# Optimization experiments

Hardware: AMD Instinct MI355X
Metric: run time of the kernel (lower is better)

Reference implementation:

```python
import jax, jax.numpy as jnp
import numpy as np

B, L, D, H, DK = 4, 256, 512, 8, 64
NEG_INF = 1.0e9


def setup_inputs() -> dict:
    key = jax.random.key(0)
    ks = jax.random.split(key, 12)
    s = 1.0 / np.sqrt(D)
    inp = {
        "q": jax.random.normal(ks[0], (B, L, D), jnp.float32),
        "k": jax.random.normal(ks[1], (B, L, D), jnp.float32),
        "v": jax.random.normal(ks[2], (B, L, D), jnp.float32),
        "mask": jnp.ones((B, L, L), jnp.int32),
        "Wq": jax.random.normal(ks[3], (D, D), jnp.float32) * s,
        "bq": jnp.zeros((D,), jnp.float32),
        "Wk": jax.random.normal(ks[4], (D, D), jnp.float32) * s,
        "bk": jnp.zeros((D,), jnp.float32),
        "Wv": jax.random.normal(ks[5], (D, D), jnp.float32) * s,
        "bv": jnp.zeros((D,), jnp.float32),
        "vp": jax.random.normal(ks[6], (1, H, 1, 1, DK), jnp.float32) * 0.1,
        "W0": jax.random.normal(ks[7], (D, D), jnp.float32) * s,
        "b0": jnp.zeros((D,), jnp.float32),
    }
    return inp


def reference(q, k, v, mask, Wq, bq, Wk, bk, Wv, bv, vp, W0, b0):
    # project and split heads: (B, L, D) -> (B, H, L, DK)
    qh = (q @ Wq + bq).reshape(B, L, H, DK).transpose(0, 2, 1, 3)
    kh = (k @ Wk + bk).reshape(B, L, H, DK).transpose(0, 2, 1, 3)
    vh = (v @ Wv + bv).reshape(B, L, H, DK).transpose(0, 2, 1, 3)
    # additive (Bahdanau) scoring: (B, H, Lq, Lk, DK) intermediate
    energy = jnp.tanh(qh[:, :, :, None, :] + kh[:, :, None, :, :])
    scores = jnp.sum(vp * energy, axis=-1)  # (B, H, Lq, Lk)
    scores = jnp.where(mask[:, None] == 0, -NEG_INF, scores)
    attn = jax.nn.softmax(scores, axis=-1)
    out = jnp.matmul(attn, vh)  # (B, H, Lq, DK)
    out = out.transpose(0, 2, 1, 3).reshape(B, L, D)
    return out @ W0 + b0
```

## Files before the change

### kernel.cpp

```cpp
#include <hip/hip_runtime.h>

#define LSEQ 256
#define DMODEL 512
#define NHEAD 8
#define DKH 64
#define BATCH 4

#define TWO_LOG2E 2.885390081777927f

using short8 = __attribute__((ext_vector_type(8))) short;
using f32x4  = __attribute__((ext_vector_type(4))) float;

__device__ __forceinline__ void split4(const float* f, ushort4& h, ushort4& l) {
  unsigned short hh[4], ll[4];
#pragma unroll
  for (int j = 0; j < 4; ++j) {
    unsigned int u = __float_as_uint(f[j]);
    hh[j] = (unsigned short)(u >> 16);
    float hf = __uint_as_float(u & 0xFFFF0000u);
    ll[j] = (unsigned short)(__float_as_uint(f[j] - hf) >> 16);
  }
  h = make_ushort4(hh[0], hh[1], hh[2], hh[3]);
  l = make_ushort4(ll[0], ll[1], ll[2], ll[3]);
}

__global__ __launch_bounds__(256) void prep_kernel(
    const float* __restrict__ q, const float* __restrict__ k, const float* __restrict__ v,
    const float* __restrict__ Wq, const float* __restrict__ Wk,
    const float* __restrict__ Wv, const float* __restrict__ W0,
    unsigned short* __restrict__ xhi, unsigned short* __restrict__ xlo,
    unsigned short* __restrict__ whi, unsigned short* __restrict__ wlo)
{
  const int z = blockIdx.z;
  const int tid = threadIdx.x;
  if (z < 3) {
    const float* X = (z == 0) ? q : (z == 1) ? k : v;
    const int r = blockIdx.x * 32 + (tid >> 3);
    const int c = blockIdx.y * 32 + ((tid & 7) << 2);
    float4 f = *(const float4*)&X[r * DMODEL + c];
    ushort4 h4, l4;
    split4((const float*)&f, h4, l4);
    const int base = (z * 1024 + r) * DMODEL + c;
    *(ushort4*)&xhi[base] = h4;
    *(ushort4*)&xlo[base] = l4;
  } else {
    if (blockIdx.x >= 16) return;
    const int g = z - 3;
    const float* W = (g == 0) ? Wq : (g == 1) ? Wk : (g == 2) ? Wv : W0;
    const float scale = (g < 2) ? TWO_LOG2E : 1.0f;
    const int k0 = blockIdx.x * 32, n0 = blockIdx.y * 32;
    __shared__ float tile[32][36];
    {
      const int r = tid >> 3, c = (tid & 7) << 2;
      float4 f = *(const float4*)&W[(k0 + r) * DMODEL + n0 + c];
      tile[r][c + 0] = f.x * scale;
      tile[r][c + 1] = f.y * scale;
      tile[r][c + 2] = f.z * scale;
      tile[r][c + 3] = f.w * scale;
    }
    __syncthreads();
    const int n = tid >> 3, kk = (tid & 7) << 2;
    float x[4];
#pragma unroll
    for (int j = 0; j < 4; ++j) x[j] = tile[kk + j][n];
    ushort4 h4, l4;
    split4(x, h4, l4);
    const int base = (g * DMODEL + n0 + n) * DMODEL + k0 + kk;
    *(ushort4*)&whi[base] = h4;
    *(ushort4*)&wlo[base] = l4;
  }
}

__device__ __forceinline__ void mfma_gemm(
    const unsigned short* __restrict__ xh, const unsigned short* __restrict__ xl,
    const unsigned short* __restrict__ wh, const unsigned short* __restrict__ wl,
    const float* __restrict__ bias, float bscale,
    float* __restrict__ out, int mode)
{
  __shared__ short8 ldsT[4][512];
  const int tid = threadIdx.x;
  const int lane = tid & 63, w = tid >> 6;
  const int bm0 = blockIdx.x * 64, bn0 = blockIdx.y * 64;

  const int r0 = tid >> 3, c0 = tid & 7;
  const int g0 = c0 ^ (r0 & 7);
  const int r1 = r0 + 32;
  const int g1 = c0 ^ (r1 & 7);
  const size_t offA0 = (size_t)(bm0 + r0) * DMODEL + g0 * 8;
  const size_t offA1 = (size_t)(bm0 + r1) * DMODEL + g1 * 8;
  const size_t offB0 = (size_t)(bn0 + r0) * DMODEL + g0 * 8;
  const size_t offB1 = (size_t)(bn0 + r1) * DMODEL + g1 * 8;

  const int mrb = (w >> 1) << 5, ncb = (w & 1) << 5;
  const int l15 = lane & 15, lh = lane >> 4, l7 = lane & 7;

  short8 st[8];
#define LOADS(K)                                        \
  { st[0] = *(const short8*)(xh + offA0 + (K));         \
    st[1] = *(const short8*)(xh + offA1 + (K));         \
    st[2] = *(const short8*)(xl + offA0 + (K));         \
    st[3] = *(const short8*)(xl + offA1 + (K));         \
    st[4] = *(const short8*)(wh + offB0 + (K));         \
    st[5] = *(const short8*)(wh + offB1 + (K));         \
    st[6] = *(const short8*)(wl + offB0 + (K));         \
    st[7] = *(const short8*)(wl + offB1 + (K)); }
#define WRITES                                          \
  { ldsT[0][tid] = st[0]; ldsT[0][tid + 256] = st[1];   \
    ldsT[1][tid] = st[2]; ldsT[1][tid + 256] = st[3];   \
    ldsT[2][tid] = st[4]; ldsT[2][tid + 256] = st[5];   \
    ldsT[3][tid] = st[6]; ldsT[3][tid + 256] = st[7]; }

  f32x4 acc[2][2] = {};
  LOADS(0);
  WRITES;
  __syncthreads();

  for (int t = 0; t < 8; ++t) {
    if (t < 7) LOADS((t + 1) * 64);
#pragma unroll
    for (int s = 0; s < 2; ++s) {
      const int chb = (s << 2) + lh;
      const int ra0 = (mrb + l15) * 8 + (chb ^ l7);
      const int ra1 = (mrb + 16 + l15) * 8 + (chb ^ l7);
      const int rb0 = (ncb + l15) * 8 + (chb ^ l7);
      const int rb1 = (ncb + 16 + l15) * 8 + (chb ^ l7);
      short8 a0h = ldsT[0][ra0], a0l = ldsT[1][ra0];
      short8 a1h = ldsT[0][ra1], a1l = ldsT[1][ra1];
      short8 b0h = ldsT[2][rb0], b0l = ldsT[3][rb0];
      short8 b1h = ldsT[2][rb1], b1l = ldsT[3][rb1];
#define MFMA_(A, B, C) C = __builtin_amdgcn_mfma_f32_16x16x32_bf16(A, B, C, 0, 0, 0)
      MFMA_(a0h, b0h, acc[0][0]); MFMA_(a0h, b0l, acc[0][0]); MFMA_(a0l, b0h, acc[0][0]);
      MFMA_(a0h, b1h, acc[0][1]); MFMA_(a0h, b1l, acc[0][1]); MFMA_(a0l, b1h, acc[0][1]);
      MFMA_(a1h, b0h, acc[1][0]); MFMA_(a1h, b0l, acc[1][0]); MFMA_(a1l, b0h, acc[1][0]);
      MFMA_(a1h, b1h, acc[1][1]); MFMA_(a1h, b1l, acc[1][1]); MFMA_(a1l, b1h, acc[1][1]);
#undef MFMA_
    }
    __syncthreads();
    if (t < 7) { WRITES; __syncthreads(); }
  }
#undef LOADS
#undef WRITES

  const int bm = bm0 + mrb, bn = bn0 + ncb;
#pragma unroll
  for (int mi = 0; mi < 2; ++mi)
#pragma unroll
    for (int ni = 0; ni < 2; ++ni) {
      const int C = bn + ni * 16 + l15;
      const float bv = bscale * bias[C];
#pragma unroll
      for (int e = 0; e < 4; ++e) {
        const int R = bm + mi * 16 + (lh << 2) + e;
        const float val = acc[mi][ni][e] + bv;
        if (mode == 0) {
          out[R * DMODEL + C] = val;
        } else {
          const int b = R >> 8, l = R & (LSEQ - 1);
          const int hh = C >> 6, dk = C & 63;
          if (mode == 1) out[((b * NHEAD + hh) * LSEQ + l) * DKH + dk] = val;
          else           out[((b * NHEAD + hh) * DKH + dk) * LSEQ + l] = val;
        }
      }
    }
}

__global__ __launch_bounds__(256) void proj_mfma_kernel(
    const unsigned short* __restrict__ xhi, const unsigned short* __restrict__ xlo,
    const unsigned short* __restrict__ whi, const unsigned short* __restrict__ wlo,
    const float* __restrict__ bq, const float* __restrict__ bk, const float* __restrict__ bv,
    float* __restrict__ qh, float* __restrict__ kT, float* __restrict__ vh)
{
  const int g = blockIdx.z;
  const unsigned short* xh = xhi + (size_t)g * 1024 * DMODEL;
  const unsigned short* xl = xlo + (size_t)g * 1024 * DMODEL;
  const unsigned short* wh = whi + (size_t)g * DMODEL * DMODEL;
  const unsigned short* wl = wlo + (size_t)g * DMODEL * DMODEL;
  if (g == 0)      mfma_gemm(xh, xl, wh, wl, bq, TWO_LOG2E, qh, 1);
  else if (g == 1) mfma_gemm(xh, xl, wh, wl, bk, TWO_LOG2E, kT, 2);
  else             mfma_gemm(xh, xl, wh, wl, bv, 1.0f, vh, 1);
}

__global__ __launch_bounds__(256) void outproj_mfma_kernel(
    const unsigned short* __restrict__ aoh, const unsigned short* __restrict__ aol,
    const unsigned short* __restrict__ whi, const unsigned short* __restrict__ wlo,
    const float* __restrict__ b0, float* __restrict__ out)
{
  mfma_gemm(aoh, aol, whi + (size_t)3 * DMODEL * DMODEL,
            wlo + (size_t)3 * DMODEL * DMODEL, b0, 1.0f, out, 0);
}

__global__ __launch_bounds__(512) void attn_kernel(
    const float* __restrict__ qh,
    const float* __restrict__ kT,
    const float* __restrict__ vh,
    const int* __restrict__ mask,
    const float* __restrict__ vp,
    unsigned short* __restrict__ aoh,
    unsigned short* __restrict__ aol)
{
  __shared__ float ksh[DKH][LSEQ];
  __shared__ float vsh[LSEQ][DKH];
  __shared__ float qsh[32][DKH];
  __shared__ float psh[8][LSEQ];
  __shared__ float vpsh[DKH];

  const int bh = blockIdx.x;
  const int b = bh >> 3, h = bh & 7;
  const int i0 = blockIdx.y * 32;
  const int tid = threadIdx.x;
  const int lane = tid & 63, w = tid >> 6;

  const float* kbase = kT + (size_t)bh * DKH * LSEQ;
  for (int t = tid; t < DKH * LSEQ / 4; t += 512) {
    const int d = t >> 6, j4 = (t & 63) << 2;
    *(float4*)&ksh[d][j4] = *(const float4*)&kbase[d * LSEQ + j4];
  }
  const float* vbase = vh + (size_t)bh * LSEQ * DKH;
  for (int t = tid; t < LSEQ * DKH / 4; t += 512) {
    const int j = t >> 4, d4 = (t & 15) << 2;
    *(float4*)&vsh[j][d4] = *(const float4*)&vbase[j * DKH + d4];
  }
  {
    const float* qbase = qh + ((size_t)bh * LSEQ + i0) * DKH;
    const int r = tid >> 4, d4 = (tid & 15) << 2;
    *(float4*)&qsh[r][d4] = *(const float4*)&qbase[r * DKH + d4];
  }
  if (tid < DKH) vpsh[tid] = vp[h * DKH + tid];
  __syncthreads();

  float tj[4][4] = {};
#pragma unroll 2
  for (int g = 0; g < 16; ++g) {
    float kv[16];
#pragma unroll
    for (int t = 0; t < 4; ++t)
#pragma unroll
      for (int c = 0; c < 4; ++c)
        kv[t * 4 + c] = ksh[(g << 2) + t][(c << 6) + lane];
    float vpv[4];
    *(float4*)vpv = *(const float4*)&vpsh[g << 2];
#pragma unroll
    for (int r = 0; r < 4; ++r) {
      float q_[4];
      *(float4*)q_ = *(const float4*)&qsh[(w << 2) + r][g << 2];
#pragma unroll
      for (int t = 0; t < 4; ++t)
#pragma unroll
        for (int c = 0; c < 4; ++c) {
          const float x = q_[t] + kv[t * 4 + c];
          const float e = __builtin_amdgcn_exp2f(x);
          tj[r][c] = fmaf(vpv[t], __builtin_amdgcn_rcpf(e + 1.f), tj[r][c]);
        }
    }
  }

  const int cg = lane >> 4, qq = lane & 15;
#pragma unroll
  for (int r = 0; r < 4; ++r) {
    const int i = i0 + (w << 2) + r;
    const int* mrow = mask + ((size_t)b * LSEQ + i) * LSEQ;
    float t4[4];
#pragma unroll
    for (int c = 0; c < 4; ++c) {
      const int mv = mrow[(c << 6) + lane];
      t4[c] = mv ? tj[r][c] : 1.0e9f;
    }
    float m = fminf(fminf(t4[0], t4[1]), fminf(t4[2], t4[3]));
#pragma unroll
    for (int off = 32; off; off >>= 1) m = fminf(m, __shfl_xor(m, off));
    const float m2 = m * TWO_LOG2E;
    float p[4];
    float sum = 0.f;
#pragma unroll
    for (int c = 0; c < 4; ++c) {
      p[c] = __builtin_amdgcn_exp2f(fmaf(t4[c], -TWO_LOG2E, m2));
      sum += p[c];
    }
#pragma unroll
    for (int off = 32; off; off >>= 1) sum += __shfl_xor(sum, off);
    const float rs = __builtin_amdgcn_rcpf(sum);
#pragma unroll
    for (int c = 0; c < 4; ++c) psh[w][(c << 6) + lane] = p[c];

    float o[4] = {0.f, 0.f, 0.f, 0.f};
#pragma unroll 4
    for (int jg = 0; jg < 16; ++jg) {
      float pv[4];
      *(float4*)pv = *(const float4*)&psh[w][(cg << 6) + (jg << 2)];
#pragma unroll
      for (int t = 0; t < 4; ++t) {
        float v_[4];
        *(float4*)v_ = *(const float4*)&vsh[(cg << 6) + (jg << 2) + t][qq << 2];
#pragma unroll
        for (int u = 0; u < 4; ++u) o[u] = fmaf(pv[t], v_[u], o[u]);
      }
    }
#pragma unroll
    for (int off = 16; off <= 32; off <<= 1) {
#pragma unroll
      for (int u = 0; u < 4; ++u) o[u] += __shfl_xor(o[u], off);
    }
    if (lane < 16) {
      float ov[4];
#pragma unroll
      for (int u = 0; u < 4; ++u) ov[u] = o[u] * rs;
      ushort4 h4, l4;
      split4(ov, h4, l4);
      const int base = ((size_t)b * LSEQ + i) * DMODEL + h * DKH + (qq << 2);
      *(ushort4*)&aoh[base] = h4;
      *(ushort4*)&aol[base] = l4;
    }
  }
}

extern "C" void kernel_launch(void* const* d_in, const int* in_sizes, int n_in,
                              void* d_out, int out_size, void* d_ws, size_t ws_size,
                              hipStream_t stream) {
  const float* q   = (const float*)d_in[0];
  const float* k   = (const float*)d_in[1];
  const float* v   = (const float*)d_in[2];
  const int*  mask = (const int*)d_in[3];
  const float* Wq  = (const float*)d_in[4];
  const float* bq  = (const float*)d_in[5];
  const float* Wk  = (const float*)d_in[6];
  const float* bk  = (const float*)d_in[7];
  const float* Wv  = (const float*)d_in[8];
  const float* bv  = (const float*)d_in[9];
  const float* vp  = (const float*)d_in[10];
  const float* W0  = (const float*)d_in[11];
  const float* b0  = (const float*)d_in[12];
  float* outp = (float*)d_out;

  char* wsb = (char*)d_ws;
  unsigned short* whi = (unsigned short*)(wsb);
  unsigned short* wlo = (unsigned short*)(wsb + (2u << 20));
  unsigned short* xhi = (unsigned short*)(wsb + (4u << 20));
  unsigned short* xlo = (unsigned short*)(wsb + (7u << 20));
  float* qh = (float*)(wsb + (10u << 20));
  float* kT = (float*)(wsb + (12u << 20));
  float* vh = (float*)(wsb + (14u << 20));
  unsigned short* aoh = xhi;
  unsigned short* aol = xlo;

  prep_kernel<<<dim3(32, 16, 7), 256, 0, stream>>>(q, k, v, Wq, Wk, Wv, W0,
                                                   xhi, xlo, whi, wlo);
  proj_mfma_kernel<<<dim3(16, 8, 3), 256, 0, stream>>>(xhi, xlo, whi, wlo,
                                                       bq, bk, bv, qh, kT, vh);
  attn_kernel<<<dim3(32, 8), 512, 0, stream>>>(qh, kT, vh, mask, vp, aoh, aol);
  outproj_mfma_kernel<<<dim3(16, 8), 256, 0, stream>>>(aoh, aol, whi, wlo, b0, outp);
}
```

Baseline: 142.0 us.

## Fuse activation bf16 splitting into GEMMs, double-buffer LDS, widen attention blocks

The activation hi/lo bf16 split moves out of the prep kernel and into the GEMM tile loaders, which now read fp32 inputs directly and split them in registers. This removes the extra write and read of the split activation arrays. The GEMM LDS is double-buffered so one sync per k-step suffices, and block indices are remapped to change the order in which tiles are scheduled. The attention kernel goes to 1024 threads with 2 rows per wave and writes fp32 output, at the cost of redundant splitting across N-tiles and larger LDS use.

```diff
diff --git a/kernel.cpp b/kernel.cpp
--- a/kernel.cpp
+++ b/kernel.cpp
@@ -24,97 +24,96 @@
   l = make_ushort4(ll[0], ll[1], ll[2], ll[3]);
 }
 
-__global__ __launch_bounds__(256) void prep_kernel(
-    const float* __restrict__ q, const float* __restrict__ k, const float* __restrict__ v,
+__device__ __forceinline__ void split8(float4 f0, float4 f1, short8& h, short8& l) {
+  float f[8] = {f0.x, f0.y, f0.z, f0.w, f1.x, f1.y, f1.z, f1.w};
+#pragma unroll
+  for (int j = 0; j < 8; ++j) {
+    unsigned int u = __float_as_uint(f[j]);
+    h[j] = (short)(u >> 16);
+    float hf = __uint_as_float(u & 0xFFFF0000u);
+    l[j] = (short)(__float_as_uint(f[j] - hf) >> 16);
+  }
+}
+
+__global__ __launch_bounds__(256) void prep_w_kernel(
     const float* __restrict__ Wq, const float* __restrict__ Wk,
     const float* __restrict__ Wv, const float* __restrict__ W0,
-    unsigned short* __restrict__ xhi, unsigned short* __restrict__ xlo,
     unsigned short* __restrict__ whi, unsigned short* __restrict__ wlo)
 {
-  const int z = blockIdx.z;
   const int tid = threadIdx.x;
-  if (z < 3) {
-    const float* X = (z == 0) ? q : (z == 1) ? k : v;
-    const int r = blockIdx.x * 32 + (tid >> 3);
-    const int c = blockIdx.y * 32 + ((tid & 7) << 2);
-    float4 f = *(const float4*)&X[r * DMODEL + c];
-    ushort4 h4, l4;
-    split4((const float*)&f, h4, l4);
-    const int base = (z * 1024 + r) * DMODEL + c;
-    *(ushort4*)&xhi[base] = h4;
-    *(ushort4*)&xlo[base] = l4;
-  } else {
-    if (blockIdx.x >= 16) return;
-    const int g = z - 3;
-    const float* W = (g == 0) ? Wq : (g == 1) ? Wk : (g == 2) ? Wv : W0;
-    const float scale = (g < 2) ? TWO_LOG2E : 1.0f;
-    const int k0 = blockIdx.x * 32, n0 = blockIdx.y * 32;
-    __shared__ float tile[32][36];
-    {
-      const int r = tid >> 3, c = (tid & 7) << 2;
-      float4 f = *(const float4*)&W[(k0 + r) * DMODEL + n0 + c];
-      tile[r][c + 0] = f.x * scale;
-      tile[r][c + 1] = f.y * scale;
-      tile[r][c + 2] = f.z * scale;
-      tile[r][c + 3] = f.w * scale;
-    }
-    __syncthreads();
-    const int n = tid >> 3, kk = (tid & 7) << 2;
-    float x[4];
-#pragma unroll
-    for (int j = 0; j < 4; ++j) x[j] = tile[kk + j][n];
-    ushort4 h4, l4;
-    split4(x, h4, l4);
-    const int base = (g * DMODEL + n0 + n) * DMODEL + k0 + kk;
-    *(ushort4*)&whi[base] = h4;
-    *(ushort4*)&wlo[base] = l4;
-  }
-}
-
-__device__ __forceinline__ void mfma_gemm(
-    const unsigned short* __restrict__ xh, const unsigned short* __restrict__ xl,
+  const int g = blockIdx.z;
+  const float* W = (g == 0) ? Wq : (g == 1) ? Wk : (g == 2) ? Wv : W0;
+  const float scale = (g < 2) ? TWO_LOG2E : 1.0f;
+  const int k0 = blockIdx.x * 32, n0 = blockIdx.y * 32;
+  __shared__ float tile[32][36];
+  {
+    const int r = tid >> 3, c = (tid & 7) << 2;
+    float4 f = *(const float4*)&W[(k0 + r) * DMODEL + n0 + c];
+    tile[r][c + 0] = f.x * scale;
+    tile[r][c + 1] = f.y * scale;
+    tile[r][c + 2] = f.z * scale;
+    tile[r][c + 3] = f.w * scale;
+  }
+  __syncthreads();
+  const int n = tid >> 3, kk = (tid & 7) << 2;
+  float x[4];
+#pragma unroll
+  for (int j = 0; j < 4; ++j) x[j] = tile[kk + j][n];
+  ushort4 h4, l4;
+  split4(x, h4, l4);
+  const int base = (g * DMODEL + n0 + n) * DMODEL + k0 + kk;
+  *(ushort4*)&whi[base] = h4;
+  *(ushort4*)&wlo[base] = l4;
+}
+
+__device__ __forceinline__ void gemm_fp32A(
+    const float* __restrict__ X,
     const unsigned short* __restrict__ wh, const unsigned short* __restrict__ wl,
     const float* __restrict__ bias, float bscale,
-    float* __restrict__ out, int mode)
-{
-  __shared__ short8 ldsT[4][512];
+    float* __restrict__ out, int mode, int bx, int by)
+{
+  __shared__ short8 lds[2][4][512];
   const int tid = threadIdx.x;
   const int lane = tid & 63, w = tid >> 6;
-  const int bm0 = blockIdx.x * 64, bn0 = blockIdx.y * 64;
-
-  const int r0 = tid >> 3, c0 = tid & 7;
-  const int g0 = c0 ^ (r0 & 7);
-  const int r1 = r0 + 32;
-  const int g1 = c0 ^ (r1 & 7);
-  const size_t offA0 = (size_t)(bm0 + r0) * DMODEL + g0 * 8;
-  const size_t offA1 = (size_t)(bm0 + r1) * DMODEL + g1 * 8;
-  const size_t offB0 = (size_t)(bn0 + r0) * DMODEL + g0 * 8;
-  const size_t offB1 = (size_t)(bn0 + r1) * DMODEL + g1 * 8;
+  const int bm0 = bx * 64, bn0 = by * 64;
+
+  const int r0 = tid >> 3, c0 = tid & 7, g0 = c0 ^ (r0 & 7);
+  const int r1 = r0 + 32,  g1 = c0 ^ (r1 & 7);
+  const size_t aoff0 = (size_t)(bm0 + r0) * DMODEL + g0 * 8;
+  const size_t aoff1 = (size_t)(bm0 + r1) * DMODEL + g1 * 8;
+  const size_t boff0 = (size_t)(bn0 + r0) * DMODEL + g0 * 8;
+  const size_t boff1 = (size_t)(bn0 + r1) * DMODEL + g1 * 8;
 
   const int mrb = (w >> 1) << 5, ncb = (w & 1) << 5;
   const int l15 = lane & 15, lh = lane >> 4, l7 = lane & 7;
 
-  short8 st[8];
-#define LOADS(K)                                        \
-  { st[0] = *(const short8*)(xh + offA0 + (K));         \
-    st[1] = *(const short8*)(xh + offA1 + (K));         \
-    st[2] = *(const short8*)(xl + offA0 + (K));         \
-    st[3] = *(const short8*)(xl + offA1 + (K));         \
-    st[4] = *(const short8*)(wh + offB0 + (K));         \
-    st[5] = *(const short8*)(wh + offB1 + (K));         \
-    st[6] = *(const short8*)(wl + offB0 + (K));         \
-    st[7] = *(const short8*)(wl + offB1 + (K)); }
-#define WRITES                                          \
-  { ldsT[0][tid] = st[0]; ldsT[0][tid + 256] = st[1];   \
-    ldsT[1][tid] = st[2]; ldsT[1][tid + 256] = st[3];   \
-    ldsT[2][tid] = st[4]; ldsT[2][tid + 256] = st[5];   \
-    ldsT[3][tid] = st[6]; ldsT[3][tid + 256] = st[7]; }
+  float4 af00, af01, af10, af11;
+  short8 b0h, b0l, b1h, b1l;
+
+#define LOADS(K)                                                  \
+  { af00 = *(const float4*)(X + aoff0 + (K));                     \
+    af01 = *(const float4*)(X + aoff0 + (K) + 4);                 \
+    af10 = *(const float4*)(X + aoff1 + (K));                     \
+    af11 = *(const float4*)(X + aoff1 + (K) + 4);                 \
+    b0h = *(const short8*)(wh + boff0 + (K));                     \
+    b0l = *(const short8*)(wl + boff0 + (K));                     \
+    b1h = *(const short8*)(wh + boff1 + (K));                     \
+    b1l = *(const short8*)(wl + boff1 + (K)); }
+#define WRITES(BUF)                                               \
+  { short8 h_, l_;                                                \
+    split8(af00, af01, h_, l_);                                   \
+    lds[BUF][0][tid] = h_; lds[BUF][1][tid] = l_;                 \
+    split8(af10, af11, h_, l_);                                   \
+    lds[BUF][0][tid + 256] = h_; lds[BUF][1][tid + 256] = l_;     \
+    lds[BUF][2][tid] = b0h; lds[BUF][3][tid] = b0l;               \
+    lds[BUF][2][tid + 256] = b1h; lds[BUF][3][tid + 256] = b1l; }
 
   f32x4 acc[2][2] = {};
   LOADS(0);
-  WRITES;
+  WRITES(0);
   __syncthreads();
 
+  int cur = 0;
   for (int t = 0; t < 8; ++t) {
     if (t < 7) LOADS((t + 1) * 64);
 #pragma unroll
@@ -124,19 +123,20 @@
       const int ra1 = (mrb + 16 + l15) * 8 + (chb ^ l7);
       const int rb0 = (ncb + l15) * 8 + (chb ^ l7);
       const int rb1 = (ncb + 16 + l15) * 8 + (chb ^ l7);
-      short8 a0h = ldsT[0][ra0], a0l = ldsT[1][ra0];
-      short8 a1h = ldsT[0][ra1], a1l = ldsT[1][ra1];
-      short8 b0h = ldsT[2][rb0], b0l = ldsT[3][rb0];
-      short8 b1h = ldsT[2][rb1], b1l = ldsT[3][rb1];
+      short8 a0h = lds[cur][0][ra0], a0l = lds[cur][1][ra0];
+      short8 a1h = lds[cur][0][ra1], a1l = lds[cur][1][ra1];
+      short8 w0h = lds[cur][2][rb0], w0l = lds[cur][3][rb0];
+      short8 w1h = lds[cur][2][rb1], w1l = lds[cur][3][rb1];
 #define MFMA_(A, B, C) C = __builtin_amdgcn_mfma_f32_16x16x32_bf16(A, B, C, 0, 0, 0)
-      MFMA_(a0h, b0h, acc[0][0]); MFMA_(a0h, b0l, acc[0][0]); MFMA_(a0l, b0h, acc[0][0]);
-      MFMA_(a0h, b1h, acc[0][1]); MFMA_(a0h, b1l, acc[0][1]); MFMA_(a0l, b1h, acc[0][1]);
-      MFMA_(a1h, b0h, acc[1][0]); MFMA_(a1h, b0l, acc[1][0]); MFMA_(a1l, b0h, acc[1][0]);
-      MFMA_(a1h, b1h, acc[1][1]); MFMA_(a1h, b1l, acc[1][1]); MFMA_(a1l, b1h, acc[1][1]);
+      MFMA_(a0h, w0h, acc[0][0]); MFMA_(a0h, w0l, acc[0][0]); MFMA_(a0l, w0h, acc[0][0]);
+      MFMA_(a0h, w1h, acc[0][1]); MFMA_(a0h, w1l, acc[0][1]); MFMA_(a0l, w1h, acc[0][1]);
+      MFMA_(a1h, w0h, acc[1][0]); MFMA_(a1h, w0l, acc[1][0]); MFMA_(a1l, w0h, acc[1][0]);
+      MFMA_(a1h, w1h, acc[1][1]); MFMA_(a1h, w1l, acc[1][1]); MFMA_(a1l, w1h, acc[1][1]);
 #undef MFMA_
     }
+    if (t < 7) WRITES(cur ^ 1);
     __syncthreads();
-    if (t < 7) { WRITES; __syncthreads(); }
+    cur ^= 1;
   }
 #undef LOADS
 #undef WRITES
@@ -165,43 +165,45 @@
 }
 
 __global__ __launch_bounds__(256) void proj_mfma_kernel(
-    const unsigned short* __restrict__ xhi, const unsigned short* __restrict__ xlo,
+    const float* __restrict__ q, const float* __restrict__ k, const float* __restrict__ v,
     const unsigned short* __restrict__ whi, const unsigned short* __restrict__ wlo,
     const float* __restrict__ bq, const float* __restrict__ bk, const float* __restrict__ bv,
     float* __restrict__ qh, float* __restrict__ kT, float* __restrict__ vh)
 {
-  const int g = blockIdx.z;
-  const unsigned short* xh = xhi + (size_t)g * 1024 * DMODEL;
-  const unsigned short* xl = xlo + (size_t)g * 1024 * DMODEL;
+  int lin = blockIdx.x + 16 * blockIdx.y + 128 * blockIdx.z;
+  lin = (lin & 7) * 48 + (lin >> 3);
+  const int bx = lin & 15, by = (lin >> 4) & 7, g = lin >> 7;
   const unsigned short* wh = whi + (size_t)g * DMODEL * DMODEL;
   const unsigned short* wl = wlo + (size_t)g * DMODEL * DMODEL;
-  if (g == 0)      mfma_gemm(xh, xl, wh, wl, bq, TWO_LOG2E, qh, 1);
-  else if (g == 1) mfma_gemm(xh, xl, wh, wl, bk, TWO_LOG2E, kT, 2);
-  else             mfma_gemm(xh, xl, wh, wl, bv, 1.0f, vh, 1);
+  if (g == 0)      gemm_fp32A(q, wh, wl, bq, TWO_LOG2E, qh, 1, bx, by);
+  else if (g == 1) gemm_fp32A(k, wh, wl, bk, TWO_LOG2E, kT, 2, bx, by);
+  else             gemm_fp32A(v, wh, wl, bv, 1.0f, vh, 1, bx, by);
 }
 
 __global__ __launch_bounds__(256) void outproj_mfma_kernel(
-    const unsigned short* __restrict__ aoh, const unsigned short* __restrict__ aol,
+    const float* __restrict__ ao,
     const unsigned short* __restrict__ whi, const unsigned short* __restrict__ wlo,
     const float* __restrict__ b0, float* __restrict__ out)
 {
-  mfma_gemm(aoh, aol, whi + (size_t)3 * DMODEL * DMODEL,
-            wlo + (size_t)3 * DMODEL * DMODEL, b0, 1.0f, out, 0);
-}
-
-__global__ __launch_bounds__(512) void attn_kernel(
+  int lin = blockIdx.x + 16 * blockIdx.y;
+  lin = (lin & 7) * 16 + (lin >> 3);
+  const int bx = lin & 15, by = lin >> 4;
+  gemm_fp32A(ao, whi + (size_t)3 * DMODEL * DMODEL,
+             wlo + (size_t)3 * DMODEL * DMODEL, b0, 1.0f, out, 0, bx, by);
+}
+
+__global__ __launch_bounds__(1024, 4) void attn_kernel(
     const float* __restrict__ qh,
     const float* __restrict__ kT,
     const float* __restrict__ vh,
     const int* __restrict__ mask,
     const float* __restrict__ vp,
-    unsigned short* __restrict__ aoh,
-    unsigned short* __restrict__ aol)
+    float* __restrict__ ao)
 {
   __shared__ float ksh[DKH][LSEQ];
   __shared__ float vsh[LSEQ][DKH];
   __shared__ float qsh[32][DKH];
-  __shared__ float psh[8][LSEQ];
+  __shared__ float psh[16][LSEQ];
   __shared__ float vpsh[DKH];
 
   const int bh = blockIdx.x;
@@ -211,16 +213,16 @@
   const int lane = tid & 63, w = tid >> 6;
 
   const float* kbase = kT + (size_t)bh * DKH * LSEQ;
-  for (int t = tid; t < DKH * LSEQ / 4; t += 512) {
+  for (int t = tid; t < DKH * LSEQ / 4; t += 1024) {
     const int d = t >> 6, j4 = (t & 63) << 2;
     *(float4*)&ksh[d][j4] = *(const float4*)&kbase[d * LSEQ + j4];
   }
   const float* vbase = vh + (size_t)bh * LSEQ * DKH;
-  for (int t = tid; t < LSEQ * DKH / 4; t += 512) {
+  for (int t = tid; t < LSEQ * DKH / 4; t += 1024) {
     const int j = t >> 4, d4 = (t & 15) << 2;
     *(float4*)&vsh[j][d4] = *(const float4*)&vbase[j * DKH + d4];
   }
-  {
+  if (tid < 512) {
     const float* qbase = qh + ((size_t)bh * LSEQ + i0) * DKH;
     const int r = tid >> 4, d4 = (tid & 15) << 2;
     *(float4*)&qsh[r][d4] = *(const float4*)&qbase[r * DKH + d4];
@@ -228,7 +230,7 @@
   if (tid < DKH) vpsh[tid] = vp[h * DKH + tid];
   __syncthreads();
 
-  float tj[4][4] = {};
+  float tj[2][4] = {};
 #pragma unroll 2
   for (int g = 0; g < 16; ++g) {
     float kv[16];
@@ -240,9 +242,9 @@
     float vpv[4];
     *(float4*)vpv = *(const float4*)&vpsh[g << 2];
 #pragma unroll
-    for (int r = 0; r < 4; ++r) {
+    for (int r = 0; r < 2; ++r) {
       float q_[4];
-      *(float4*)q_ = *(const float4*)&qsh[(w << 2) + r][g << 2];
+      *(float4*)q_ = *(const float4*)&qsh[(w << 1) + r][g << 2];
 #pragma unroll
       for (int t = 0; t < 4; ++t)
 #pragma unroll
@@ -256,8 +258,8 @@
 
   const int cg = lane >> 4, qq = lane & 15;
 #pragma unroll
-  for (int r = 0; r < 4; ++r) {
-    const int i = i0 + (w << 2) + r;
+  for (int r = 0; r < 2; ++r) {
+    const int i = i0 + (w << 1) + r;
     const int* mrow = mask + ((size_t)b * LSEQ + i) * LSEQ;
     float t4[4];
 #pragma unroll
@@ -304,11 +306,8 @@
       float ov[4];
 #pragma unroll
       for (int u = 0; u < 4; ++u) ov[u] = o[u] * rs;
-      ushort4 h4, l4;
-      split4(ov, h4, l4);
-      const int base = ((size_t)b * LSEQ + i) * DMODEL + h * DKH + (qq << 2);
-      *(ushort4*)&aoh[base] = h4;
-      *(ushort4*)&aol[base] = l4;
+      *(float4*)&ao[((size_t)b * LSEQ + i) * DMODEL + h * DKH + (qq << 2)] =
+          *(float4*)ov;
     }
   }
 }
@@ -334,18 +333,14 @@
   char* wsb = (char*)d_ws;
   unsigned short* whi = (unsigned short*)(wsb);
   unsigned short* wlo = (unsigned short*)(wsb + (2u << 20));
-  unsigned short* xhi = (unsigned short*)(wsb + (4u << 20));
-  unsigned short* xlo = (unsigned short*)(wsb + (7u << 20));
-  float* qh = (float*)(wsb + (10u << 20));
-  float* kT = (float*)(wsb + (12u << 20));
-  float* vh = (float*)(wsb + (14u << 20));
-  unsigned short* aoh = xhi;
-  unsigned short* aol = xlo;
-
-  prep_kernel<<<dim3(32, 16, 7), 256, 0, stream>>>(q, k, v, Wq, Wk, Wv, W0,
-                                                   xhi, xlo, whi, wlo);
-  proj_mfma_kernel<<<dim3(16, 8, 3), 256, 0, stream>>>(xhi, xlo, whi, wlo,
+  float* qh = (float*)(wsb + (4u << 20));
+  float* kT = (float*)(wsb + (6u << 20));
+  float* vh = (float*)(wsb + (8u << 20));
+  float* ao = (float*)(wsb + (10u << 20));
+
+  prep_w_kernel<<<dim3(16, 16, 4), 256, 0, stream>>>(Wq, Wk, Wv, W0, whi, wlo);
+  proj_mfma_kernel<<<dim3(16, 8, 3), 256, 0, stream>>>(q, k, v, whi, wlo,
                                                        bq, bk, bv, qh, kT, vh);
-  attn_kernel<<<dim3(32, 8), 512, 0, stream>>>(qh, kT, vh, mask, vp, aoh, aol);
-  outproj_mfma_kernel<<<dim3(16, 8), 256, 0, stream>>>(aoh, aol, whi, wlo, b0, outp);
-}
+  attn_kernel<<<dim3(32, 8), 1024, 0, stream>>>(qh, kT, vh, mask, vp, ao);
+  outproj_mfma_kernel<<<dim3(16, 8), 256, 0, stream>>>(ao, whi, wlo, b0, outp);
+}
```

After: 139.7 us. About the same (-1.6%).
